# Optimization experiments

Measured on AMD Instinct MI355X. Metric: run time of the kernel, lower is better.

## Reference

```python
import jax, jax.numpy as jnp
import numpy as np

N = 3072          # num nodes
H = 256           # hidden_features
B = 4             # num_heads
HD = H // B       # per-head dim
PRIOR_MU = 1.0
PRIOR_SIGMA = 1.0
LN_EPS = 1e-5


def setup_inputs() -> dict:
    key = jax.random.key(0)
    ks = jax.random.split(key, 12)
    s = 0.02  # weight init scale
    return {
        "h": jax.random.normal(ks[0], (N, H), jnp.float32),
        "gamma": jnp.ones((H,), jnp.float32),
        "beta": jnp.zeros((H,), jnp.float32),
        "W_k": jax.random.normal(ks[1], (H, H), jnp.float32) * s,
        "b_k": jnp.zeros((H,), jnp.float32),
        "W_mu": jax.random.normal(ks[2], (H, H), jnp.float32) * s,
        "b_mu": jnp.zeros((H,), jnp.float32),
        "W_ls": jax.random.normal(ks[3], (H, H), jnp.float32) * s,
        "b_ls": jnp.zeros((H,), jnp.float32),
        "W_v": jax.random.normal(ks[4], (H * B, H), jnp.float32) * s,
        "b_v": jnp.zeros((H,), jnp.float32),
        "diffusion": jax.random.uniform(ks[5], (N, N, 1), jnp.float32),
        "eps": jax.random.normal(ks[6], (N, N, B), jnp.float32),
    }


def reference(h, gamma, beta, W_k, b_k, W_mu, b_mu, W_ls, b_ls, W_v, b_v, diffusion, eps):
    h0 = h
    # LayerNorm
    mean = jnp.mean(h, axis=-1, keepdims=True)
    var = jnp.var(h, axis=-1, keepdims=True)
    hn = (h - mean) * jax.lax.rsqrt(var + LN_EPS) * gamma + beta
    # Q/K-style projections, split into heads: [N, HD, B]
    k = (hn @ W_k + b_k).reshape(N, HD, B)
    mu = (hn @ W_mu + b_mu).reshape(N, HD, B)
    ls = (hn @ W_ls + b_ls).reshape(N, HD, B)
    scale = HD ** -0.5
    mu = jnp.einsum('xyb,zyb->xzb', k, mu) * scale       # [N, N, B]
    ls = jnp.einsum('xyb,zyb->xzb', k, ls) * scale       # [N, N, B]
    sigma = jax.nn.softplus(ls)
    # KL(LogNormal(mu, sigma) || LogNormal(log(prior_mu), prior_sigma))
    mu_p = jnp.log(jnp.asarray(PRIOR_MU, h.dtype))
    sig_p = jnp.asarray(PRIOR_SIGMA, h.dtype)
    kl = (jnp.log(sig_p / sigma)
          + (sigma ** 2 + (mu - mu_p) ** 2) / (2.0 * sig_p ** 2)
          - 0.5)
    kl = (kl * jnp.sign(diffusion)).sum(-1).mean()
    # reparameterized LogNormal sample, masked by diffusion matrix
    a = jnp.exp(mu + sigma * eps) * diffusion            # [N, N, B]
    # L1 normalize over source-node axis (dim=-2), torch F.normalize semantics
    denom = jnp.clip(jnp.sum(jnp.abs(a), axis=-2, keepdims=True), 1e-12)
    a = a / denom
    # diffusion-weighted aggregation: [N, B, H] -> [N, B*H]
    out = jnp.einsum('xyb,yz->xbz', a, hn).reshape(N, B * H)
    out = out @ W_v + b_v                                 # fc_v (dropout = eval mode)
    out = jax.nn.elu(out) + h0
    return out, kl
```

## Files before the change

kernel.cpp:

```cpp
#include <hip/hip_runtime.h>
#include <hip/hip_bf16.h>


#define NN 3072
#define HH 256
#define NB 4
#define HD 64
constexpr int KMLSZ = 192 * 2 * 64 * 8;

typedef __attribute__((ext_vector_type(8))) short bf16x8;
typedef __attribute__((ext_vector_type(4))) float f32x4;

static __device__ inline short f2bf(float f) {
    __hip_bfloat16 h = __float2bfloat16(f);
    return __builtin_bit_cast(short, h);
}

__global__ void k0_prep(const float* __restrict__ Wk, const float* __restrict__ Wmu,
                        const float* __restrict__ Wls, const float* __restrict__ bk,
                        const float* __restrict__ bmu, const float* __restrict__ bls,
                        const float* __restrict__ Wv, short* __restrict__ WTcat,
                        float* __restrict__ biascat, short* __restrict__ WvT,
                        float* __restrict__ denom) {
    __shared__ float t[64][65];
    int bx = blockIdx.x;
    if (bx < 48) {
        int mat = bx >> 4;
        int by = (bx >> 2) & 3, bc = bx & 3;
        int y0 = by * 64, c0 = bc * 64;
        const float* W = (mat == 0) ? Wk : (mat == 1 ? Wmu : Wls);
        float scale = (mat == 0) ? 0.125f : 1.f;
        int r = threadIdx.x >> 4, c4 = (threadIdx.x & 15) * 4;
#pragma unroll
        for (int i = 0; i < 4; i++) {
            int yl = r + i * 16;
            float4 v = *(const float4*)(W + (y0 + yl) * 256 + c0 + c4);
            t[yl][c4] = v.x; t[yl][c4 + 1] = v.y; t[yl][c4 + 2] = v.z; t[yl][c4 + 3] = v.w;
        }
        __syncthreads();
#pragma unroll
        for (int i = 0; i < 4; i++) {
            int cl = r + i * 16;
            int corig = c0 + cl;
            int cp = mat * 256 + (corig & 3) * 64 + (corig >> 2);
            short4 v = make_short4(f2bf(t[c4][cl] * scale), f2bf(t[c4 + 1][cl] * scale),
                                   f2bf(t[c4 + 2][cl] * scale), f2bf(t[c4 + 3][cl] * scale));
            *(short4*)(WTcat + cp * 256 + y0 + c4) = v;
        }
        return;
    }
    if (bx < 112) {
        int b = bx - 48;
        int bk2 = b >> 2, bn = b & 3;
        int k0 = bk2 * 64, n0 = bn * 64;
        int r = threadIdx.x >> 4, c4 = (threadIdx.x & 15) * 4;
#pragma unroll
        for (int i = 0; i < 4; i++) {
            int kk = r + i * 16;
            float4 v = *(const float4*)(Wv + (k0 + kk) * 256 + n0 + c4);
            t[kk][c4] = v.x; t[kk][c4 + 1] = v.y; t[kk][c4 + 2] = v.z; t[kk][c4 + 3] = v.w;
        }
        __syncthreads();
#pragma unroll
        for (int i = 0; i < 4; i++) {
            int nn = r + i * 16;
            short4 v = make_short4(f2bf(t[c4][nn]), f2bf(t[c4 + 1][nn]),
                                   f2bf(t[c4 + 2][nn]), f2bf(t[c4 + 3][nn]));
            *(short4*)(WvT + (n0 + nn) * 1024 + k0 + c4) = v;
        }
        return;
    }
    if (bx == 112) {
        int cc = threadIdx.x;
        int corig = (cc & 63) * 4 + (cc >> 6);
        biascat[cc] = bk[corig] * 0.125f;
        biascat[256 + cc] = bmu[corig];
        biascat[512 + cc] = bls[corig];
        return;
    }
    int i = (bx - 113) * 256 + threadIdx.x;
    if (i < 13312) denom[i] = 0.f;
}

__global__ void k1_ln(const float* __restrict__ h, const float* __restrict__ gamma,
                      const float* __restrict__ beta, short* __restrict__ hn) {
    int row = blockIdx.x, tid = threadIdx.x;
    float v = h[row * 256 + tid];
    float s = v, s2 = v * v;
    for (int off = 32; off; off >>= 1) {
        s += __shfl_xor(s, off);
        s2 += __shfl_xor(s2, off);
    }
    __shared__ float red[8];
    int w = tid >> 6, lane = tid & 63;
    if (!lane) { red[w] = s; red[4 + w] = s2; }
    __syncthreads();
    s = red[0] + red[1] + red[2] + red[3];
    s2 = red[4] + red[5] + red[6] + red[7];
    float mean = s * (1.f / 256.f);
    float var = s2 * (1.f / 256.f) - mean * mean;
    float rs = rsqrtf(var + 1e-5f);
    hn[row * 256 + tid] = f2bf((v - mean) * rs * gamma[tid] + beta[tid]);
}

__global__ void k1b_tr(const short* __restrict__ hn, short* __restrict__ hnT) {
    __shared__ short t[64][68];
    int bn = blockIdx.x >> 2, bh = blockIdx.x & 3;
    int n0 = bn * 64, h0 = bh * 64;
    int r = threadIdx.x >> 4, c4 = (threadIdx.x & 15) * 4;
#pragma unroll
    for (int i = 0; i < 4; i++) {
        int nn = r + i * 16;
        *(short4*)&t[nn][c4] = *(const short4*)(hn + (n0 + nn) * 256 + h0 + c4);
    }
    __syncthreads();
#pragma unroll
    for (int i = 0; i < 4; i++) {
        int hh = r + i * 16;
        short4 v = make_short4(t[c4][hh], t[c4 + 1][hh], t[c4 + 2][hh], t[c4 + 3][hh]);
        *(short4*)(hnT + (h0 + hh) * NN + n0 + c4) = v;
    }
}

__global__ __launch_bounds__(256) void k2_proj(const short* __restrict__ hn,
                                               const short* __restrict__ WTcat,
                                               const float* __restrict__ biascat,
                                               short* __restrict__ kml) {
    int bx = blockIdx.x;
    int mt = bx / 12, nb = bx % 12;
    int m0 = mt * 64, n0 = nb * 64;
    int tid = threadIdx.x, w = tid >> 6, lane = tid & 63, q = lane >> 4, c = lane & 15;
    int mrow = m0 + w * 16;
    f32x4 acc[4] = {{0, 0, 0, 0}, {0, 0, 0, 0}, {0, 0, 0, 0}, {0, 0, 0, 0}};
    for (int k0 = 0; k0 < 256; k0 += 32) {
        bf16x8 af = *(const bf16x8*)(hn + (mrow + c) * 256 + k0 + q * 8);
#pragma unroll
        for (int nt = 0; nt < 4; nt++) {
            bf16x8 bf = *(const bf16x8*)(WTcat + (n0 + nt * 16 + c) * 256 + k0 + q * 8);
            acc[nt] = __builtin_amdgcn_mfma_f32_16x16x32_bf16(af, bf, acc[nt], 0, 0, 0);
        }
    }
#pragma unroll
    for (int nt = 0; nt < 4; nt++) {
        int cp = n0 + nt * 16 + c;
        float bias = biascat[cp];
        int mat = cp >> 8, b = (cp >> 6) & 3, y = cp & 63;
        short* dst = kml + (size_t)(mat * 4 + b) * KMLSZ;
        int kh2 = y >> 5, lq = (y >> 3) & 3, j = y & 7;
        int zt = mt * 4 + w;
#pragma unroll
        for (int r = 0; r < 4; r++) {
            int ml = 4 * q + r;
            dst[(((zt * 2 + kh2) * 64) + lq * 16 + ml) * 8 + j] = f2bf(acc[nt][r] + bias);
        }
    }
}

__global__ __launch_bounds__(256) void k3a_elem(
    const short* __restrict__ kml, const float* __restrict__ eps,
    const float* __restrict__ diff, short* __restrict__ apk,
    float* __restrict__ denom, float* __restrict__ klsum) {
    __shared__ float klred[4];
    const int tid = threadIdx.x;
    const int w = tid >> 6, lane = tid & 63, q = lane >> 4, c = lane & 15;
    const int xb = blockIdx.x % 48;
    const int zc = blockIdx.x / 48;
    const int xt = xb * 4 + w;
    const int x0 = xt * 16;

    bf16x8 qf[NB][2];
#pragma unroll
    for (int b = 0; b < NB; b++)
#pragma unroll
        for (int kh = 0; kh < 2; kh++)
            qf[b][kh] = *(const bf16x8*)(kml + (size_t)b * KMLSZ +
                                         ((xt * 2 + kh) * 64 + lane) * 8);

    float den_acc[NB] = {0.f, 0.f, 0.f, 0.f};
    float kl_acc = 0.f;
    const size_t xrow = (size_t)(x0 + c) * NN;

    f32x4 e_nxt[4];
    float d_nxt[4];
    {
        const int z16 = zc * 64;
#pragma unroll
        for (int r = 0; r < 4; r++) {
            e_nxt[r] = __builtin_nontemporal_load(
                (const f32x4*)(eps + (xrow + (size_t)(z16 + 4 * q + r)) * 4));
            d_nxt[r] = __builtin_nontemporal_load(diff + xrow + z16 + 4 * q + r);
        }
    }

#pragma unroll
    for (int t = 0; t < 4; t++) {
        const int zt2 = zc * 4 + t;
        f32x4 e4[4];
        float dif[4];
#pragma unroll
        for (int r = 0; r < 4; r++) { e4[r] = e_nxt[r]; dif[r] = d_nxt[r]; }
        if (t < 3) {
            const int z16 = (zt2 + 1) * 16;
#pragma unroll
            for (int r = 0; r < 4; r++) {
                e_nxt[r] = __builtin_nontemporal_load(
                    (const f32x4*)(eps + (xrow + (size_t)(z16 + 4 * q + r)) * 4));
                d_nxt[r] = __builtin_nontemporal_load(diff + xrow + z16 + 4 * q + r);
            }
        }
#pragma unroll
        for (int b = 0; b < NB; b++) {
            const short* mup = kml + (size_t)(NB + b) * KMLSZ;
            const short* lsp = kml + (size_t)(2 * NB + b) * KMLSZ;
            bf16x8 a0 = *(const bf16x8*)(mup + ((zt2 * 2 + 0) * 64 + lane) * 8);
            bf16x8 a1 = *(const bf16x8*)(mup + ((zt2 * 2 + 1) * 64 + lane) * 8);
            bf16x8 l0 = *(const bf16x8*)(lsp + ((zt2 * 2 + 0) * 64 + lane) * 8);
            bf16x8 l1 = *(const bf16x8*)(lsp + ((zt2 * 2 + 1) * 64 + lane) * 8);
            f32x4 smu = {0.f, 0.f, 0.f, 0.f};
            smu = __builtin_amdgcn_mfma_f32_16x16x32_bf16(a0, qf[b][0], smu, 0, 0, 0);
            smu = __builtin_amdgcn_mfma_f32_16x16x32_bf16(a1, qf[b][1], smu, 0, 0, 0);
            f32x4 sls = {0.f, 0.f, 0.f, 0.f};
            sls = __builtin_amdgcn_mfma_f32_16x16x32_bf16(l0, qf[b][0], sls, 0, 0, 0);
            sls = __builtin_amdgcn_mfma_f32_16x16x32_bf16(l1, qf[b][1], sls, 0, 0, 0);
            short pk[4];
#pragma unroll
            for (int r = 0; r < 4; r++) {
                float mu = smu[r];
                float ls = sls[r];
                float e = e4[r][b];
                float d = dif[r];
                float ex = __expf(-fabsf(ls));
                float sg = fmaxf(ls, 0.f) + __logf(1.f + ex);
                float kle = -__logf(sg) + 0.5f * (sg * sg + mu * mu) - 0.5f;
                float sgn = (d > 0.f) ? 1.f : ((d < 0.f) ? -1.f : 0.f);
                kl_acc += sgn * kle;
                float av = __expf(mu + sg * e) * d;
                den_acc[b] += fabsf(av);
                pk[r] = f2bf(av);
            }
            *(short4*)(apk + (((size_t)b * 192 + xt) * 192 + zt2) * 256 + c * 16 + q * 4) =
                make_short4(pk[0], pk[1], pk[2], pk[3]);
        }
    }
#pragma unroll
    for (int b = 0; b < NB; b++) {
        float d = den_acc[b];
        d += __shfl_down(d, 32);
        d += __shfl_down(d, 16);
        if (q == 0) atomicAdd(&denom[(x0 + c) * NB + b], d);
    }
    for (int off = 32; off; off >>= 1) kl_acc += __shfl_xor(kl_acc, off);
    if (lane == 0) klred[w] = kl_acc;
    __syncthreads();
    if (tid == 0) atomicAdd(klsum, klred[0] + klred[1] + klred[2] + klred[3]);
}

__global__ __launch_bounds__(256) void k3b_agg(
    const short* __restrict__ apk, const short* __restrict__ hnT,
    const float* __restrict__ denom, short* __restrict__ aggn) {
    __shared__ float red[2][64 * 33];
    const int tid = threadIdx.x;
    const int w = tid >> 6, lane = tid & 63, q = lane >> 4, c = lane & 15;
    const int kw = w >> 1, nw = w & 1;
    const int bid = blockIdx.x;
    const int b = bid & 3;
    const int nb = (bid >> 2) & 3;
    const int mb = bid >> 4;
    const int m0 = mb * 64;
    const int n0 = nb * 64 + nw * 32;
    const int q2 = q >> 1, q1 = q & 1;

    f32x4 acc[4][2];
#pragma unroll
    for (int i = 0; i < 4; i++)
#pragma unroll
        for (int j = 0; j < 2; j++) acc[i][j] = (f32x4){0.f, 0.f, 0.f, 0.f};

    const size_t abase = ((size_t)b * 192 + mb * 4) * 192 * 256;
    for (int ks = 0; ks < 48; ks++) {
        const int kglob = kw * 1536 + ks * 32;
        const int T2 = kw * 96 + ks * 2;
        bf16x8 af[4], bf[2];
#pragma unroll
        for (int mt = 0; mt < 4; mt++)
            af[mt] = __builtin_nontemporal_load(
                (const bf16x8*)(apk + abase + (size_t)(mt * 192 + T2 + q2) * 256 +
                                c * 16 + q1 * 8));
#pragma unroll
        for (int nt = 0; nt < 2; nt++)
            bf[nt] = *(const bf16x8*)(hnT + (size_t)(n0 + nt * 16 + c) * NN + kglob + q * 8);
#pragma unroll
        for (int mt = 0; mt < 4; mt++)
#pragma unroll
            for (int nt = 0; nt < 2; nt++)
                acc[mt][nt] = __builtin_amdgcn_mfma_f32_16x16x32_bf16(
                    af[mt], bf[nt], acc[mt][nt], 0, 0, 0);
    }

    if (kw == 1) {
#pragma unroll
        for (int mt = 0; mt < 4; mt++)
#pragma unroll
            for (int nt = 0; nt < 2; nt++)
#pragma unroll
                for (int r = 0; r < 4; r++)
                    red[nw][(mt * 16 + 4 * q + r) * 33 + nt * 16 + c] = acc[mt][nt][r];
    }
    __syncthreads();
    if (kw == 0) {
#pragma unroll
        for (int mt = 0; mt < 4; mt++)
#pragma unroll
            for (int r = 0; r < 4; r++) {
                int x = m0 + mt * 16 + 4 * q + r;
                float rcp = 1.f / fmaxf(denom[x * 4 + b], 1e-12f);
#pragma unroll
                for (int nt = 0; nt < 2; nt++) {
                    float s = acc[mt][nt][r] + red[nw][(mt * 16 + 4 * q + r) * 33 + nt * 16 + c];
                    aggn[(size_t)x * 1024 + b * 256 + n0 + nt * 16 + c] = f2bf(s * rcp);
                }
            }
    }
}

__global__ __launch_bounds__(256) void k4_out(const short* __restrict__ aggn,
                                              const short* __restrict__ WvT,
                                              const float* __restrict__ bv,
                                              const float* __restrict__ h,
                                              const float* __restrict__ klsum,
                                              float* __restrict__ out) {
    int bx = blockIdx.x;
    int mt = bx >> 2, nb = bx & 3;
    int m0 = mt * 64, n0 = nb * 64;
    int tid = threadIdx.x, w = tid >> 6, lane = tid & 63, q = lane >> 4, c = lane & 15;
    int mrow = m0 + w * 16;
    f32x4 acc[4] = {{0, 0, 0, 0}, {0, 0, 0, 0}, {0, 0, 0, 0}, {0, 0, 0, 0}};
    for (int k0 = 0; k0 < 1024; k0 += 32) {
        bf16x8 af = *(const bf16x8*)(aggn + (mrow + c) * 1024 + k0 + q * 8);
#pragma unroll
        for (int nt = 0; nt < 4; nt++) {
            bf16x8 bf = *(const bf16x8*)(WvT + (n0 + nt * 16 + c) * 1024 + k0 + q * 8);
            acc[nt] = __builtin_amdgcn_mfma_f32_16x16x32_bf16(af, bf, acc[nt], 0, 0, 0);
        }
    }
#pragma unroll
    for (int nt = 0; nt < 4; nt++) {
        int col = n0 + nt * 16 + c;
        float bias = bv[col];
#pragma unroll
        for (int r = 0; r < 4; r++) {
            int row = mrow + 4 * q + r;
            float v = acc[nt][r] + bias;
            v = (v > 0.f) ? v : (__expf(v) - 1.f);
            out[row * 256 + col] = v + h[row * 256 + col];
        }
    }
    if (bx == 0 && tid == 0) out[786432] = klsum[0] * (1.0f / 9437184.0f);
}

extern "C" void kernel_launch(void* const* d_in, const int* in_sizes, int n_in,
                              void* d_out, int out_size, void* d_ws, size_t ws_size,
                              hipStream_t stream) {
    const float* h = (const float*)d_in[0];
    const float* gamma = (const float*)d_in[1];
    const float* beta = (const float*)d_in[2];
    const float* Wk = (const float*)d_in[3];
    const float* bk = (const float*)d_in[4];
    const float* Wmu = (const float*)d_in[5];
    const float* bmu = (const float*)d_in[6];
    const float* Wls = (const float*)d_in[7];
    const float* bls = (const float*)d_in[8];
    const float* Wv = (const float*)d_in[9];
    const float* bv = (const float*)d_in[10];
    const float* diff = (const float*)d_in[11];
    const float* eps = (const float*)d_in[12];
    float* out = (float*)d_out;

    char* p = (char*)d_ws;
    short* apk = (short*)p;    p += (size_t)75497472;
    float* denom = (float*)p;  p += 49152;
    float* klsum = (float*)p;  p += 4096;
    short* hn = (short*)p;     p += 1572864;
    short* hnT = (short*)p;    p += 1572864;
    short* kml = (short*)p;    p += 4718592;
    short* WTcat = (short*)p;  p += 393216;
    float* biasc = (float*)p;  p += 4096;
    short* WvT = (short*)p;    p += 524288;
    short* aggn = (short*)p;

    k0_prep<<<165, 256, 0, stream>>>(Wk, Wmu, Wls, bk, bmu, bls, Wv, WTcat, biasc, WvT,
                                     denom);
    k1_ln<<<3072, 256, 0, stream>>>(h, gamma, beta, hn);
    k1b_tr<<<192, 256, 0, stream>>>(hn, hnT);
    k2_proj<<<576, 256, 0, stream>>>(hn, WTcat, biasc, kml);
    k3a_elem<<<48 * 48, 256, 0, stream>>>(kml, eps, diff, apk, denom, klsum);
    k3b_agg<<<48 * 4 * 4, 256, 0, stream>>>(apk, hnT, denom, aggn);
    k4_out<<<192, 256, 0, stream>>>(aggn, WvT, bv, h, klsum, out);
}
```

Baseline: 463.9 us.

## Retile aggregation GEMM to full-K per wave with double-buffered loads; swizzle elem blocks

The aggregation kernel now has each block cover 32 rows by all 256 columns for one head. Each wave owns 64 columns over the full K range, which removes the split-K shared-memory reduction and the barrier. Operand loads are software-pipelined with two register buffers, and the A tile is read once per block instead of once per column block. The elementwise kernel also remaps block IDs with an XCD-style swizzle so neighbouring z-chunks share a chiplet. In exchange, the grid drops to 384 blocks, which means less parallelism and a longer serial K loop per wave.

```diff
diff --git a/kernel.cpp b/kernel.cpp
--- a/kernel.cpp
+++ b/kernel.cpp
@@ -163,8 +163,9 @@
     __shared__ float klred[4];
     const int tid = threadIdx.x;
     const int w = tid >> 6, lane = tid & 63, q = lane >> 4, c = lane & 15;
-    const int xb = blockIdx.x % 48;
-    const int zc = blockIdx.x / 48;
+    const int swz = (blockIdx.x & 7) * 288 + (blockIdx.x >> 3);
+    const int xb = swz % 48;
+    const int zc = swz / 48;
     const int xt = xb * 4 + w;
     const int x0 = xt * 16;
 
@@ -258,69 +259,70 @@
 __global__ __launch_bounds__(256) void k3b_agg(
     const short* __restrict__ apk, const short* __restrict__ hnT,
     const float* __restrict__ denom, short* __restrict__ aggn) {
-    __shared__ float red[2][64 * 33];
     const int tid = threadIdx.x;
     const int w = tid >> 6, lane = tid & 63, q = lane >> 4, c = lane & 15;
-    const int kw = w >> 1, nw = w & 1;
+    const int q2 = q >> 1, q1 = q & 1;
     const int bid = blockIdx.x;
     const int b = bid & 3;
-    const int nb = (bid >> 2) & 3;
-    const int mb = bid >> 4;
-    const int m0 = mb * 64;
-    const int n0 = nb * 64 + nw * 32;
-    const int q2 = q >> 1, q1 = q & 1;
-
-    f32x4 acc[4][2];
-#pragma unroll
-    for (int i = 0; i < 4; i++)
-#pragma unroll
-        for (int j = 0; j < 2; j++) acc[i][j] = (f32x4){0.f, 0.f, 0.f, 0.f};
-
-    const size_t abase = ((size_t)b * 192 + mb * 4) * 192 * 256;
-    for (int ks = 0; ks < 48; ks++) {
-        const int kglob = kw * 1536 + ks * 32;
-        const int T2 = kw * 96 + ks * 2;
-        bf16x8 af[4], bf[2];
-#pragma unroll
-        for (int mt = 0; mt < 4; mt++)
-            af[mt] = __builtin_nontemporal_load(
-                (const bf16x8*)(apk + abase + (size_t)(mt * 192 + T2 + q2) * 256 +
-                                c * 16 + q1 * 8));
-#pragma unroll
-        for (int nt = 0; nt < 2; nt++)
-            bf[nt] = *(const bf16x8*)(hnT + (size_t)(n0 + nt * 16 + c) * NN + kglob + q * 8);
-#pragma unroll
-        for (int mt = 0; mt < 4; mt++)
-#pragma unroll
-            for (int nt = 0; nt < 2; nt++)
-                acc[mt][nt] = __builtin_amdgcn_mfma_f32_16x16x32_bf16(
-                    af[mt], bf[nt], acc[mt][nt], 0, 0, 0);
-    }
-
-    if (kw == 1) {
-#pragma unroll
-        for (int mt = 0; mt < 4; mt++)
-#pragma unroll
-            for (int nt = 0; nt < 2; nt++)
-#pragma unroll
-                for (int r = 0; r < 4; r++)
-                    red[nw][(mt * 16 + 4 * q + r) * 33 + nt * 16 + c] = acc[mt][nt][r];
-    }
-    __syncthreads();
-    if (kw == 0) {
-#pragma unroll
-        for (int mt = 0; mt < 4; mt++)
-#pragma unroll
-            for (int r = 0; r < 4; r++) {
-                int x = m0 + mt * 16 + 4 * q + r;
-                float rcp = 1.f / fmaxf(denom[x * 4 + b], 1e-12f);
-#pragma unroll
-                for (int nt = 0; nt < 2; nt++) {
-                    float s = acc[mt][nt][r] + red[nw][(mt * 16 + 4 * q + r) * 33 + nt * 16 + c];
-                    aggn[(size_t)x * 1024 + b * 256 + n0 + nt * 16 + c] = f2bf(s * rcp);
-                }
-            }
-    }
+    const int mb = bid >> 2;
+    const int m0 = mb * 32;
+    const int n0 = w * 64;
+
+    f32x4 acc[2][4];
+#pragma unroll
+    for (int i = 0; i < 2; i++)
+#pragma unroll
+        for (int j = 0; j < 4; j++) acc[i][j] = (f32x4){0.f, 0.f, 0.f, 0.f};
+
+    const short* abase = apk + ((size_t)b * 192 + mb * 2) * 192 * 256 + c * 16 + q1 * 8;
+    const short* bbase = hnT + (size_t)(n0 + c) * NN + q * 8;
+
+#define LDA(KS, MT) (*(const bf16x8*)(abase + (size_t)((MT)*192 + (KS)*2 + q2) * 256))
+#define LDB(KS, NT) (*(const bf16x8*)(bbase + (size_t)(NT)*16 * NN + (KS)*32))
+#define PREF(AF, BF, KS)                                       \
+    do {                                                       \
+        AF##0 = LDA(KS, 0); AF##1 = LDA(KS, 1);                \
+        BF##0 = LDB(KS, 0); BF##1 = LDB(KS, 1);                \
+        BF##2 = LDB(KS, 2); BF##3 = LDB(KS, 3);                \
+    } while (0)
+#define MFMA8(AF, BF)                                                           \
+    do {                                                                        \
+        acc[0][0] = __builtin_amdgcn_mfma_f32_16x16x32_bf16(AF##0, BF##0, acc[0][0], 0, 0, 0); \
+        acc[0][1] = __builtin_amdgcn_mfma_f32_16x16x32_bf16(AF##0, BF##1, acc[0][1], 0, 0, 0); \
+        acc[0][2] = __builtin_amdgcn_mfma_f32_16x16x32_bf16(AF##0, BF##2, acc[0][2], 0, 0, 0); \
+        acc[0][3] = __builtin_amdgcn_mfma_f32_16x16x32_bf16(AF##0, BF##3, acc[0][3], 0, 0, 0); \
+        acc[1][0] = __builtin_amdgcn_mfma_f32_16x16x32_bf16(AF##1, BF##0, acc[1][0], 0, 0, 0); \
+        acc[1][1] = __builtin_amdgcn_mfma_f32_16x16x32_bf16(AF##1, BF##1, acc[1][1], 0, 0, 0); \
+        acc[1][2] = __builtin_amdgcn_mfma_f32_16x16x32_bf16(AF##1, BF##2, acc[1][2], 0, 0, 0); \
+        acc[1][3] = __builtin_amdgcn_mfma_f32_16x16x32_bf16(AF##1, BF##3, acc[1][3], 0, 0, 0); \
+    } while (0)
+
+    bf16x8 afA0, afA1, bfA0, bfA1, bfA2, bfA3;
+    bf16x8 afB0, afB1, bfB0, bfB1, bfB2, bfB3;
+    PREF(afA, bfA, 0);
+    PREF(afB, bfB, 1);
+    for (int ks = 0; ks < 96; ks += 2) {
+        MFMA8(afA, bfA);
+        if (ks + 2 < 96) PREF(afA, bfA, ks + 2);
+        MFMA8(afB, bfB);
+        if (ks + 3 < 96) PREF(afB, bfB, ks + 3);
+    }
+#undef LDA
+#undef LDB
+#undef PREF
+#undef MFMA8
+
+#pragma unroll
+    for (int mt = 0; mt < 2; mt++)
+#pragma unroll
+        for (int r = 0; r < 4; r++) {
+            int x = m0 + mt * 16 + 4 * q + r;
+            float rcp = 1.f / fmaxf(denom[x * 4 + b], 1e-12f);
+#pragma unroll
+            for (int nt = 0; nt < 4; nt++)
+                aggn[(size_t)x * 1024 + b * 256 + n0 + nt * 16 + c] =
+                    f2bf(acc[mt][nt][r] * rcp);
+        }
 }
 
 __global__ __launch_bounds__(256) void k4_out(const short* __restrict__ aggn,
@@ -394,6 +396,6 @@
     k1b_tr<<<192, 256, 0, stream>>>(hn, hnT);
     k2_proj<<<576, 256, 0, stream>>>(hn, WTcat, biasc, kml);
     k3a_elem<<<48 * 48, 256, 0, stream>>>(kml, eps, diff, apk, denom, klsum);
-    k3b_agg<<<48 * 4 * 4, 256, 0, stream>>>(apk, hnT, denom, aggn);
+    k3b_agg<<<384, 256, 0, stream>>>(apk, hnT, denom, aggn);
     k4_out<<<192, 256, 0, stream>>>(aggn, WvT, bv, h, klsum, out);
 }
```

Measured after the change: 471.4 us. No clear change (+1.6%).
